# Kernel optimization log

Measured on AMD Instinct MI355X. Metric: run time of the kernel, lower is better.

The kernel has to match this reference:

```python
import jax, jax.numpy as jnp
import numpy as np

R = 7            # radius
STRIDE = 2       # downsample_factor
K_SIDE = 2 * R + 1   # 15 -> K = 225 neighbors


def setup_inputs() -> dict:
    key = jax.random.key(0)
    B, H, W = 8, 512, 512
    # integer segment labels in [0, 64), stored as float32
    segments = jax.random.randint(key, (B, 1, H, W), 0, 64).astype(jnp.float32)
    return {"segments": segments}


def _local_equality_adj(segments):
    # segments: [B, 1, H_full, W_full]
    seg = segments[..., ::STRIDE, ::STRIDE]          # [B, 1, H, W]
    B, _, H, W = seg.shape
    x = seg[:, 0]                                    # [B, H, W]
    # zero-pad borders by R (unfold-style neighborhood extraction)
    padded = jnp.pad(x, ((0, 0), (R, R), (R, R)))    # [B, H+2R, W+2R]
    offs = jnp.arange(K_SIDE)
    dy, dx = jnp.meshgrid(offs, offs, indexing="ij")
    dy = dy.reshape(-1)                              # [K]
    dx = dx.reshape(-1)                              # [K]

    def gather(dy_i, dx_i):
        return jax.lax.dynamic_slice(padded, (0, dy_i, dx_i), (B, H, W))

    neighbors = jax.vmap(gather)(dy, dx)             # [K, B, H, W]
    neighbors = jnp.transpose(neighbors, (1, 0, 2, 3))  # [B, K, H, W]
    # broadcast equality: center [B,1,H,W] vs neighbors [B,K,H,W]
    adj = (seg == neighbors).astype(jnp.float32)     # [B, K, H, W]
    return adj


def reference(segments):
    return _local_equality_adj(segments)
```

## Files before the change

kernel.cpp:

```cpp
#include <hip/hip_runtime.h>


#define RAD 7
#define KS 15
#define HW 256
#define IN_W 512
#define TILE_W (HW + 2 * RAD)
#define TILE_PITCH 272

__global__ __launch_bounds__(256) void adj_kernel(const float* __restrict__ in,
                                                  float* __restrict__ out) {
    __shared__ float smem[KS][TILE_PITCH];

    const int y   = blockIdx.x;
    const int b   = blockIdx.y;
    const int tid = threadIdx.x;

    const float* inb = in + (size_t)b * (IN_W * IN_W);

    #pragma unroll
    for (int r = 0; r < KS; ++r) {
        const int gy = y - RAD + r;
        for (int c = tid; c < TILE_W; c += 256) {
            const int gx = c - RAD;
            float v = 0.0f;
            if ((unsigned)gy < HW && (unsigned)gx < HW) {
                v = inb[(size_t)(2 * gy) * IN_W + 2 * gx];
            }
            smem[r][c] = v;
        }
    }
    __syncthreads();

    const int x = tid;
    const float s = smem[RAD][x + RAD];

    float* op = out + (size_t)b * 225 * (HW * HW) + (size_t)y * HW + x;

    #pragma unroll
    for (int r = 0; r < KS; ++r) {
        #pragma unroll
        for (int dc = 0; dc < KS; ++dc) {
            const float n = smem[r][x + dc];
            *op = (s == n) ? 1.0f : 0.0f;
            op += HW * HW;
        }
    }
}

extern "C" void kernel_launch(void* const* d_in, const int* in_sizes, int n_in,
                              void* d_out, int out_size, void* d_ws, size_t ws_size,
                              hipStream_t stream) {
    const float* segments = (const float*)d_in[0];
    float* out = (float*)d_out;
    dim3 grid(HW, 8);
    dim3 block(256);
    adj_kernel<<<grid, block, 0, stream>>>(segments, out);
}
```

Measured before the change: 472.0 us.

## Vectorize outputs to float4 per lane and split kernel rows across waves

Each lane now computes four adjacent output pixels and writes them with 16-byte nontemporal stores. It reads a 20-float window from shared memory with vector loads instead of issuing 15 scalar LDS reads per row. The 15 kernel rows are distributed across the 4 wavefronts of the block, and the smem fill now also covers the padding columns up to the pitch. This is meant to cut store instruction count and improve write coalescing on a store-bandwidth-bound kernel. The cost is an uneven row split, with some waves doing 4 rows and others 3.

```diff
diff --git a/kernel.cpp b/kernel.cpp
--- a/kernel.cpp
+++ b/kernel.cpp
@@ -7,6 +7,9 @@
 #define IN_W 512
 #define TILE_W (HW + 2 * RAD)
 #define TILE_PITCH 272
+#define PLANE (HW * HW)
+
+typedef float vf4 __attribute__((ext_vector_type(4)));
 
 __global__ __launch_bounds__(256) void adj_kernel(const float* __restrict__ in,
                                                   float* __restrict__ out) {
@@ -21,7 +24,7 @@
     #pragma unroll
     for (int r = 0; r < KS; ++r) {
         const int gy = y - RAD + r;
-        for (int c = tid; c < TILE_W; c += 256) {
+        for (int c = tid; c < TILE_PITCH; c += 256) {
             const int gx = c - RAD;
             float v = 0.0f;
             if ((unsigned)gy < HW && (unsigned)gx < HW) {
@@ -32,18 +35,39 @@
     }
     __syncthreads();
 
-    const int x = tid;
-    const float s = smem[RAD][x + RAD];
+    const int wv   = tid >> 6;
+    const int lane = tid & 63;
+    const int x    = lane * 4;
 
-    float* op = out + (size_t)b * 225 * (HW * HW) + (size_t)y * HW + x;
+    const float s0 = smem[RAD][x + RAD + 0];
+    const float s1 = smem[RAD][x + RAD + 1];
+    const float s2 = smem[RAD][x + RAD + 2];
+    const float s3 = smem[RAD][x + RAD + 3];
 
-    #pragma unroll
-    for (int r = 0; r < KS; ++r) {
+    float* base = out + (size_t)b * (KS * KS * (size_t)PLANE) + (size_t)y * HW + x;
+
+    for (int r = wv; r < KS; r += 4) {
+        const float* rowp = &smem[r][x];
+        vf4 w0 = *(const vf4*)(rowp + 0);
+        vf4 w1 = *(const vf4*)(rowp + 4);
+        vf4 w2 = *(const vf4*)(rowp + 8);
+        vf4 w3 = *(const vf4*)(rowp + 12);
+        vf4 w4 = *(const vf4*)(rowp + 16);
+        float win[20] = { w0.x, w0.y, w0.z, w0.w,
+                          w1.x, w1.y, w1.z, w1.w,
+                          w2.x, w2.y, w2.z, w2.w,
+                          w3.x, w3.y, w3.z, w3.w,
+                          w4.x, w4.y, w4.z, w4.w };
+        float* op = base + (size_t)(r * KS) * PLANE;
         #pragma unroll
         for (int dc = 0; dc < KS; ++dc) {
-            const float n = smem[r][x + dc];
-            *op = (s == n) ? 1.0f : 0.0f;
-            op += HW * HW;
+            vf4 v;
+            v.x = (s0 == win[dc + 0]) ? 1.0f : 0.0f;
+            v.y = (s1 == win[dc + 1]) ? 1.0f : 0.0f;
+            v.z = (s2 == win[dc + 2]) ? 1.0f : 0.0f;
+            v.w = (s3 == win[dc + 3]) ? 1.0f : 0.0f;
+            __builtin_nontemporal_store(v, (vf4*)op);
+            op += PLANE;
         }
     }
 }
```

Result: no change. 463.8 us (-1.7%).

## Stage padded downsampled image in workspace and write output planes with vector nontemporal stores

Applied to the files above, without the earlier changes.

A prep kernel writes the strided, zero-padded downsampled image into a workspace buffer. The main kernel is reorganised so each block owns one neighbor offset and a quarter of one output plane, and each thread handles four columns. It reads the center and shifted neighbor straight from the workspace (which should stay cache-resident) and writes contiguous float4 results with nontemporal stores. This aims to make the store-bound output fully coalesced and vectorised, at the cost of an extra kernel launch and unaligned vector loads for the neighbor.

```diff
diff --git a/kernel.cpp b/kernel.cpp
--- a/kernel.cpp
+++ b/kernel.cpp
@@ -5,46 +5,61 @@
 #define KS 15
 #define HW 256
 #define IN_W 512
-#define TILE_W (HW + 2 * RAD)
-#define TILE_PITCH 272
+#define P_PITCH 272
+#define P_OFF 8
+#define IMG_P (P_PITCH * P_PITCH)
+#define PLANE (HW * HW)
 
-__global__ __launch_bounds__(256) void adj_kernel(const float* __restrict__ in,
+typedef float vf4  __attribute__((ext_vector_type(4)));
+typedef float vf4u __attribute__((ext_vector_type(4), aligned(4)));
+
+__global__ __launch_bounds__(256) void prep_kernel(const float* __restrict__ in,
+                                                   float* __restrict__ staged) {
+    const int r = blockIdx.x;
+    const int b = blockIdx.y;
+    const float* inb = in + (size_t)b * (IN_W * IN_W);
+    float* row = staged + (size_t)b * IMG_P + (size_t)r * P_PITCH;
+    const int gy = r - P_OFF;
+    for (int c = threadIdx.x; c < P_PITCH; c += 256) {
+        const int gx = c - P_OFF;
+        float v = 0.0f;
+        if ((unsigned)gy < HW && (unsigned)gx < HW)
+            v = inb[(size_t)(2 * gy) * IN_W + 2 * gx];
+        row[c] = v;
+    }
+}
+
+__global__ __launch_bounds__(256) void adj_kernel(const float* __restrict__ staged,
                                                   float* __restrict__ out) {
-    __shared__ float smem[KS][TILE_PITCH];
+    const int kq = blockIdx.x;
+    const int b  = blockIdx.y;
+    const int k  = kq >> 2;
+    const int q  = kq & 3;
+    const int dy = k / KS - RAD;
+    const int dx = k % KS - RAD;
 
-    const int y   = blockIdx.x;
-    const int b   = blockIdx.y;
-    const int tid = threadIdx.x;
+    const int t    = threadIdx.x;
+    const int rsub = t >> 6;
+    const int col  = (t & 63) * 4;
 
-    const float* inb = in + (size_t)b * (IN_W * IN_W);
+    const float* img = staged + (size_t)b * IMG_P;
+    const float* cen = img + (size_t)(P_OFF)      * P_PITCH + (P_OFF + col);
+    const float* nbr = img + (size_t)(P_OFF + dy) * P_PITCH + (P_OFF + col + dx);
 
-    #pragma unroll
-    for (int r = 0; r < KS; ++r) {
-        const int gy = y - RAD + r;
-        for (int c = tid; c < TILE_W; c += 256) {
-            const int gx = c - RAD;
-            float v = 0.0f;
-            if ((unsigned)gy < HW && (unsigned)gx < HW) {
-                v = inb[(size_t)(2 * gy) * IN_W + 2 * gx];
-            }
-            smem[r][c] = v;
-        }
-    }
-    __syncthreads();
+    float* op = out + ((size_t)b * (KS * KS) + k) * PLANE;
 
-    const int x = tid;
-    const float s = smem[RAD][x + RAD];
-
-    float* op = out + (size_t)b * 225 * (HW * HW) + (size_t)y * HW + x;
-
-    #pragma unroll
-    for (int r = 0; r < KS; ++r) {
-        #pragma unroll
-        for (int dc = 0; dc < KS; ++dc) {
-            const float n = smem[r][x + dc];
-            *op = (s == n) ? 1.0f : 0.0f;
-            op += HW * HW;
-        }
+    const int row0 = q * 64;
+    #pragma unroll 4
+    for (int i = 0; i < 16; ++i) {
+        const int row = row0 + i * 4 + rsub;
+        vf4  c = *(const vf4*) (cen + (size_t)row * P_PITCH);
+        vf4u n = *(const vf4u*)(nbr + (size_t)row * P_PITCH);
+        vf4 v;
+        v.x = (c.x == n.x) ? 1.0f : 0.0f;
+        v.y = (c.y == n.y) ? 1.0f : 0.0f;
+        v.z = (c.z == n.z) ? 1.0f : 0.0f;
+        v.w = (c.w == n.w) ? 1.0f : 0.0f;
+        __builtin_nontemporal_store(v, (vf4*)(op + (size_t)row * HW + col));
     }
 }
 
@@ -52,8 +67,12 @@
                               void* d_out, int out_size, void* d_ws, size_t ws_size,
                               hipStream_t stream) {
     const float* segments = (const float*)d_in[0];
-    float* out = (float*)d_out;
-    dim3 grid(HW, 8);
-    dim3 block(256);
-    adj_kernel<<<grid, block, 0, stream>>>(segments, out);
+    float* out    = (float*)d_out;
+    float* staged = (float*)d_ws;
+
+    dim3 pgrid(P_PITCH, 8);
+    prep_kernel<<<pgrid, dim3(256), 0, stream>>>(segments, staged);
+
+    dim3 agrid(KS * KS * 4, 8);
+    adj_kernel<<<agrid, dim3(256), 0, stream>>>(staged, out);
 }
```

Result: no change. 466.6 us (-1.1%).
